# Performance work log

Measured on AMD Instinct MI355X. Metric: run time of the kernel, lower is better.

The kernel has to match this reference:

```python
import jax, jax.numpy as jnp
import numpy as np

BITS = 4
MAXQ = 15            # 2**BITS - 1
PACK = 32 // BITS    # 8 int4 values per int32
GROUPSIZE = 128
M, K, N = 2048, 4096, 4096
G = K // GROUPSIZE


def setup_inputs() -> dict:
    key = jax.random.key(0)
    k1, k2, k3, k4, k5 = jax.random.split(key, 5)
    x = jax.random.normal(k1, (M, K), dtype=jnp.float32)
    qweight = jax.random.randint(k2, (K // PACK, N), 0, 2147483647, dtype=jnp.int32)
    qzeros = jax.random.randint(k3, (G, N // PACK), 0, 2147483647, dtype=jnp.int32)
    scales = jax.random.uniform(k4, (G, N), dtype=jnp.float32) * 0.01
    g_idx = (jnp.arange(K, dtype=jnp.int32) // GROUPSIZE).astype(jnp.int32)
    bias = jax.random.normal(k5, (N,), dtype=jnp.float32)
    return {"x": x, "qweight": qweight, "qzeros": qzeros,
            "scales": scales, "g_idx": g_idx, "bias": bias}


def _dequantize(qweight, qzeros, scales, g_idx):
    shifts = (jnp.arange(PACK, dtype=jnp.int32) * BITS)
    # unpack weights along K: [K//8, N] -> [K//8, 8, N] -> [K, N]
    w_int = ((qweight[:, None, :] >> shifts[None, :, None]) & MAXQ)
    w_int = w_int.reshape(K, N)
    # unpack zeros along N: [G, N//8] -> [G, N//8, 8] -> [G, N]; kernel adds 1
    z_int = ((qzeros[:, :, None] >> shifts[None, None, :]) & MAXQ) + 1
    z_int = z_int.reshape(G, N)
    # group-wise dequant: W[k, n] = (w - zeros[g_idx[k]]) * scales[g_idx[k]]
    W = (w_int - z_int[g_idx]).astype(jnp.float32) * scales[g_idx]
    return W  # [K, N]


def reference(x, qweight, qzeros, scales, g_idx, bias):
    W = _dequantize(qweight, qzeros, scales, g_idx)
    return x @ W + bias  # [M, N]
```

## Files before the change

kernel.cpp:

```cpp
#include <hip/hip_runtime.h>
#include <hip/hip_bf16.h>
#include <stdint.h>

#define M_DIM 2048
#define K_DIM 4096
#define N_DIM 4096

typedef __attribute__((ext_vector_type(8))) short short8;
typedef __attribute__((ext_vector_type(4))) float f32x4;

#define MFMA __builtin_amdgcn_mfma_f32_16x16x32_bf16

__device__ __forceinline__ uint32_t bf16pk(float a, float b) {
  uint32_t ua = __float_as_uint(a);
  ua = (ua + 0x7FFFu + ((ua >> 16) & 1u)) >> 16;
  uint32_t ub = __float_as_uint(b);
  ub = (ub + 0x7FFFu + ((ub >> 16) & 1u)) >> 16;
  return ua | (ub << 16);
}

__device__ __forceinline__ void glds16(const char* g, char* l) {
  __builtin_amdgcn_global_load_lds((__attribute__((address_space(1))) void*)g,
                                   (__attribute__((address_space(3))) void*)l, 16, 0, 0);
}


__global__ void __launch_bounds__(256) cvt_x_kernel(const float* __restrict__ x,
                                                    char* __restrict__ xImg) {
  const int mt = blockIdx.x >> 6, ktp = blockIdx.x & 63;
  const int tid = threadIdx.x;
  const int row = tid & 127, sh = tid >> 7;
  const int s = ktp * 2 + sh;
  const float* src = x + (size_t)(mt * 128 + row) * K_DIM + s * 32;
  char* dst = xImg + (size_t)(mt * 128 + s) * 8192 + row * 16;
#pragma unroll
  for (int slot = 0; slot < 4; ++slot) {
    float4 f0 = *(const float4*)(src + slot * 8);
    float4 f1 = *(const float4*)(src + slot * 8 + 4);
    uint4 pk;
    pk.x = bf16pk(f0.x, f0.y);
    pk.y = bf16pk(f0.z, f0.w);
    pk.z = bf16pk(f1.x, f1.y);
    pk.w = bf16pk(f1.z, f1.w);
    *(uint4*)(dst + slot * 2048) = pk;
  }
}

__global__ void __launch_bounds__(256) deq_w_kernel(const uint32_t* __restrict__ qweight,
                                                    const uint32_t* __restrict__ qzeros,
                                                    const float* __restrict__ scales,
                                                    char* __restrict__ wImg) {
  const int nt = blockIdx.x >> 6, ktp = blockIdx.x & 63;
  const int tid = threadIdx.x;
  const int n = tid & 127, sh = tid >> 7;
  const int s = ktp * 2 + sh;
  const int g = ktp >> 1;
  const int gn = nt * 128 + n;
  uint32_t zq = qzeros[g * (N_DIM / 8) + (gn >> 3)];
  const int z = (int)((zq >> ((gn & 7) * 4)) & 15u) + 1;
  const float s_ = scales[g * N_DIM + gn];
  char* dst = wImg + (size_t)(nt * 128 + s) * 8192 + n * 16;
#pragma unroll
  for (int slot = 0; slot < 4; ++slot) {
    uint32_t q = qweight[(size_t)(s * 4 + slot) * N_DIM + gn];
    float f[8];
#pragma unroll
    for (int v = 0; v < 8; ++v) {
      int w = (int)((q >> (4 * v)) & 15u);
      f[v] = (float)(w - z) * s_;
    }
    uint4 pk;
    pk.x = bf16pk(f[0], f[1]);
    pk.y = bf16pk(f[2], f[3]);
    pk.z = bf16pk(f[4], f[5]);
    pk.w = bf16pk(f[6], f[7]);
    *(uint4*)(dst + slot * 2048) = pk;
  }
}

__global__ void __launch_bounds__(128, 2) gemm_kernel(const char* __restrict__ xImg,
                                                      const char* __restrict__ wImg,
                                                      const float* __restrict__ bias,
                                                      float* __restrict__ out,
                                                      float* __restrict__ part1) {
  __shared__ uint4 ldsv[2048];
  char* lds = (char*)ldsv;
  const int tid = threadIdx.x;
  const int lane = tid & 63, wc = tid >> 6;
  const int lr = lane & 15, lk = lane >> 4;

  const int bid = blockIdx.x;
  const int wg = (bid & 7) * 128 + (bid >> 3);
  const int mb = wg & 15, nb = (wg >> 4) & 31, ks = wg >> 9;

  f32x4 acc[8][4];
#pragma unroll
  for (int i = 0; i < 8; ++i)
#pragma unroll
    for (int j = 0; j < 4; ++j) acc[i][j] = f32x4{0.f, 0.f, 0.f, 0.f};

  const char* aT = xImg + (size_t)(mb * 128 + ks * 64) * 8192;
  const char* bT = wImg + (size_t)(nb * 128 + ks * 64) * 8192;

  int aoff[8], boff[4];
#pragma unroll
  for (int i = 0; i < 8; ++i) aoff[i] = lk * 2048 + (i * 16 + lr) * 16;
#pragma unroll
  for (int j = 0; j < 4; ++j) boff[j] = 8192 + lk * 2048 + (wc * 64 + j * 16 + lr) * 16;

#define STAGE(T, SB)                                                     \
  do {                                                                   \
    const char* sA = aT + (size_t)(T) * 8192;                            \
    const char* sB = bT + (size_t)(T) * 8192;                            \
    char* dA = lds + (SB);                                               \
    _Pragma("unroll")                                                    \
    for (int h = 0; h < 4; ++h) {                                        \
      glds16(sA + h * 2048 + tid * 16, dA + h * 2048 + tid * 16);        \
      glds16(sB + h * 2048 + tid * 16, dA + 8192 + h * 2048 + tid * 16); \
    }                                                                    \
  } while (0)

  STAGE(0, 0);
  asm volatile("s_waitcnt vmcnt(0)" ::: "memory");
  __builtin_amdgcn_sched_barrier(0);
  __builtin_amdgcn_s_barrier();

#pragma unroll 2
  for (int t = 0; t < 64; ++t) {
    const char* buf = lds + (t & 1) * 16384;
    if (t < 63) STAGE(t + 1, ((t + 1) & 1) * 16384);
    __builtin_amdgcn_sched_barrier(0);

    short8 a0 = *(const short8*)(buf + aoff[0]);
    short8 a1 = *(const short8*)(buf + aoff[1]);
    short8 a2 = *(const short8*)(buf + aoff[2]);
    short8 a3 = *(const short8*)(buf + aoff[3]);
    short8 a4 = *(const short8*)(buf + aoff[4]);
    short8 a5 = *(const short8*)(buf + aoff[5]);
    short8 a6 = *(const short8*)(buf + aoff[6]);
    short8 a7 = *(const short8*)(buf + aoff[7]);
    short8 b0 = *(const short8*)(buf + boff[0]);
    short8 b1 = *(const short8*)(buf + boff[1]);
    short8 b2 = *(const short8*)(buf + boff[2]);
    short8 b3 = *(const short8*)(buf + boff[3]);

    asm volatile("s_waitcnt lgkmcnt(3)" ::: "memory");
    __builtin_amdgcn_sched_barrier(0);
    __builtin_amdgcn_s_setprio(1);
    acc[0][0] = MFMA(a0, b0, acc[0][0], 0, 0, 0);
    acc[1][0] = MFMA(a1, b0, acc[1][0], 0, 0, 0);
    acc[2][0] = MFMA(a2, b0, acc[2][0], 0, 0, 0);
    acc[3][0] = MFMA(a3, b0, acc[3][0], 0, 0, 0);
    acc[4][0] = MFMA(a4, b0, acc[4][0], 0, 0, 0);
    acc[5][0] = MFMA(a5, b0, acc[5][0], 0, 0, 0);
    acc[6][0] = MFMA(a6, b0, acc[6][0], 0, 0, 0);
    acc[7][0] = MFMA(a7, b0, acc[7][0], 0, 0, 0);
    asm volatile("s_waitcnt lgkmcnt(2)" ::: "memory");
    __builtin_amdgcn_sched_barrier(0);
    acc[0][1] = MFMA(a0, b1, acc[0][1], 0, 0, 0);
    acc[1][1] = MFMA(a1, b1, acc[1][1], 0, 0, 0);
    acc[2][1] = MFMA(a2, b1, acc[2][1], 0, 0, 0);
    acc[3][1] = MFMA(a3, b1, acc[3][1], 0, 0, 0);
    acc[4][1] = MFMA(a4, b1, acc[4][1], 0, 0, 0);
    acc[5][1] = MFMA(a5, b1, acc[5][1], 0, 0, 0);
    acc[6][1] = MFMA(a6, b1, acc[6][1], 0, 0, 0);
    acc[7][1] = MFMA(a7, b1, acc[7][1], 0, 0, 0);
    asm volatile("s_waitcnt lgkmcnt(1)" ::: "memory");
    __builtin_amdgcn_sched_barrier(0);
    acc[0][2] = MFMA(a0, b2, acc[0][2], 0, 0, 0);
    acc[1][2] = MFMA(a1, b2, acc[1][2], 0, 0, 0);
    acc[2][2] = MFMA(a2, b2, acc[2][2], 0, 0, 0);
    acc[3][2] = MFMA(a3, b2, acc[3][2], 0, 0, 0);
    acc[4][2] = MFMA(a4, b2, acc[4][2], 0, 0, 0);
    acc[5][2] = MFMA(a5, b2, acc[5][2], 0, 0, 0);
    acc[6][2] = MFMA(a6, b2, acc[6][2], 0, 0, 0);
    acc[7][2] = MFMA(a7, b2, acc[7][2], 0, 0, 0);
    asm volatile("s_waitcnt lgkmcnt(0)" ::: "memory");
    __builtin_amdgcn_sched_barrier(0);
    acc[0][3] = MFMA(a0, b3, acc[0][3], 0, 0, 0);
    acc[1][3] = MFMA(a1, b3, acc[1][3], 0, 0, 0);
    acc[2][3] = MFMA(a2, b3, acc[2][3], 0, 0, 0);
    acc[3][3] = MFMA(a3, b3, acc[3][3], 0, 0, 0);
    acc[4][3] = MFMA(a4, b3, acc[4][3], 0, 0, 0);
    acc[5][3] = MFMA(a5, b3, acc[5][3], 0, 0, 0);
    acc[6][3] = MFMA(a6, b3, acc[6][3], 0, 0, 0);
    acc[7][3] = MFMA(a7, b3, acc[7][3], 0, 0, 0);
    __builtin_amdgcn_s_setprio(0);

    if (t < 63) {
      asm volatile("s_waitcnt vmcnt(0)" ::: "memory");
      __builtin_amdgcn_sched_barrier(0);
      __builtin_amdgcn_s_barrier();
    }
  }
#undef STAGE

  const int colB = nb * 128 + wc * 64 + lr;
  const int rowB = mb * 128 + lk * 4;
  if (part1 != nullptr) {
    float* dst = ks ? part1 : out;
#pragma unroll
    for (int j = 0; j < 4; ++j) {
      int col = colB + j * 16;
      float bj = (ks == 0) ? bias[col] : 0.f;
#pragma unroll
      for (int i = 0; i < 8; ++i) {
        int row = rowB + i * 16;
#pragma unroll
        for (int r = 0; r < 4; ++r)
          dst[(size_t)(row + r) * N_DIM + col] = acc[i][j][r] + bj;
      }
    }
  } else {
#pragma unroll
    for (int j = 0; j < 4; ++j) {
      int col = colB + j * 16;
      float bj = (ks == 0) ? bias[col] : 0.f;
#pragma unroll
      for (int i = 0; i < 8; ++i) {
        int row = rowB + i * 16;
#pragma unroll
        for (int r = 0; r < 4; ++r)
          atomicAdd(&out[(size_t)(row + r) * N_DIM + col], acc[i][j][r] + bj);
      }
    }
  }
}

__global__ void __launch_bounds__(256) reduce_kernel(float* __restrict__ out,
                                                     const float* __restrict__ part1) {
  int i = blockIdx.x * 256 + threadIdx.x;
  float4 o = ((const float4*)out)[i];
  float4 p = ((const float4*)part1)[i];
  o.x += p.x; o.y += p.y; o.z += p.z; o.w += p.w;
  ((float4*)out)[i] = o;
}

__global__ void fallback_kernel(const float* __restrict__ x, const uint32_t* __restrict__ qweight,
                                const uint32_t* __restrict__ qzeros, const float* __restrict__ scales,
                                const float* __restrict__ bias, float* __restrict__ out) {
  __shared__ float xs[16][17];
  __shared__ float ws[16][17];
  int tx = threadIdx.x, ty = threadIdx.y;
  int col = blockIdx.x * 16 + tx;
  int row = blockIdx.y * 16 + ty;
  float acc = 0.f;
  for (int k0 = 0; k0 < K_DIM; k0 += 16) {
    xs[ty][tx] = x[(size_t)row * K_DIM + k0 + tx];
    int k = k0 + ty;
    int g = k >> 7;
    uint32_t q = qweight[(size_t)(k >> 3) * N_DIM + col];
    int w = (int)((q >> ((k & 7) * 4)) & 15u);
    uint32_t zq = qzeros[g * (N_DIM / 8) + (col >> 3)];
    int z = (int)((zq >> ((col & 7) * 4)) & 15u) + 1;
    ws[ty][tx] = (float)(w - z) * scales[g * N_DIM + col];
    __syncthreads();
#pragma unroll
    for (int kk = 0; kk < 16; ++kk) acc += xs[ty][kk] * ws[kk][tx];
    __syncthreads();
  }
  out[(size_t)row * N_DIM + col] = acc + bias[col];
}

extern "C" void kernel_launch(void* const* d_in, const int* in_sizes, int n_in,
                              void* d_out, int out_size, void* d_ws, size_t ws_size,
                              hipStream_t stream) {
  const float* x = (const float*)d_in[0];
  const uint32_t* qweight = (const uint32_t*)d_in[1];
  const uint32_t* qzeros = (const uint32_t*)d_in[2];
  const float* scales = (const float*)d_in[3];
  const float* bias = (const float*)d_in[5];
  float* out = (float*)d_out;

  const size_t X_IMG = (size_t)16 * 128 * 8192;
  const size_t W_IMG = (size_t)32 * 128 * 8192;
  const size_t PART = (size_t)M_DIM * N_DIM * 4;

  if (ws_size >= X_IMG + W_IMG + PART) {
    char* xImg = (char*)d_ws;
    char* wImg = (char*)d_ws + X_IMG;
    float* part1 = (float*)((char*)d_ws + X_IMG + W_IMG);
    cvt_x_kernel<<<1024, 256, 0, stream>>>(x, xImg);
    deq_w_kernel<<<2048, 256, 0, stream>>>(qweight, qzeros, scales, wImg);
    gemm_kernel<<<1024, 128, 0, stream>>>(xImg, wImg, bias, out, part1);
    reduce_kernel<<<8192, 256, 0, stream>>>(out, part1);
  } else if (ws_size >= X_IMG + W_IMG) {
    char* xImg = (char*)d_ws;
    char* wImg = (char*)d_ws + X_IMG;
    hipMemsetAsync(out, 0, (size_t)M_DIM * N_DIM * sizeof(float), stream);
    cvt_x_kernel<<<1024, 256, 0, stream>>>(x, xImg);
    deq_w_kernel<<<2048, 256, 0, stream>>>(qweight, qzeros, scales, wImg);
    gemm_kernel<<<1024, 128, 0, stream>>>(xImg, wImg, bias, out, nullptr);
  } else {
    fallback_kernel<<<dim3(N_DIM / 16, M_DIM / 16), dim3(16, 16), 0, stream>>>(
        x, qweight, qzeros, scales, bias, out);
  }
}
```

Measured before the change: 101.0 us.

## Move split-K reduction into workgroup via LDS and merge prep kernels

The two K-halves now run as wave pairs inside one 256-thread workgroup instead of separate workgroups, with partial accumulators exchanged through LDS before the output write. This removes the fp32 partial buffer, its write and readback, and the separate reduce kernel. The x-conversion and weight-dequant kernels are also merged into one launch. In exchange the workgroup uses twice the LDS (64 KB) and the grid halves to 512 workgroups, which may reduce occupancy and latency hiding.

Result: faster. 82.42 us (-18.4%).

```diff
diff --git a/kernel.cpp b/kernel.cpp
--- a/kernel.cpp
+++ b/kernel.cpp
@@ -25,73 +25,75 @@
 }
 
 
-__global__ void __launch_bounds__(256) cvt_x_kernel(const float* __restrict__ x,
-                                                    char* __restrict__ xImg) {
-  const int mt = blockIdx.x >> 6, ktp = blockIdx.x & 63;
+__global__ void __launch_bounds__(256) prep_kernel(const float* __restrict__ x,
+                                                   const uint32_t* __restrict__ qweight,
+                                                   const uint32_t* __restrict__ qzeros,
+                                                   const float* __restrict__ scales,
+                                                   char* __restrict__ xImg,
+                                                   char* __restrict__ wImg) {
   const int tid = threadIdx.x;
-  const int row = tid & 127, sh = tid >> 7;
-  const int s = ktp * 2 + sh;
-  const float* src = x + (size_t)(mt * 128 + row) * K_DIM + s * 32;
-  char* dst = xImg + (size_t)(mt * 128 + s) * 8192 + row * 16;
-#pragma unroll
-  for (int slot = 0; slot < 4; ++slot) {
-    float4 f0 = *(const float4*)(src + slot * 8);
-    float4 f1 = *(const float4*)(src + slot * 8 + 4);
-    uint4 pk;
-    pk.x = bf16pk(f0.x, f0.y);
-    pk.y = bf16pk(f0.z, f0.w);
-    pk.z = bf16pk(f1.x, f1.y);
-    pk.w = bf16pk(f1.z, f1.w);
-    *(uint4*)(dst + slot * 2048) = pk;
-  }
-}
-
-__global__ void __launch_bounds__(256) deq_w_kernel(const uint32_t* __restrict__ qweight,
-                                                    const uint32_t* __restrict__ qzeros,
-                                                    const float* __restrict__ scales,
-                                                    char* __restrict__ wImg) {
-  const int nt = blockIdx.x >> 6, ktp = blockIdx.x & 63;
-  const int tid = threadIdx.x;
-  const int n = tid & 127, sh = tid >> 7;
-  const int s = ktp * 2 + sh;
-  const int g = ktp >> 1;
-  const int gn = nt * 128 + n;
-  uint32_t zq = qzeros[g * (N_DIM / 8) + (gn >> 3)];
-  const int z = (int)((zq >> ((gn & 7) * 4)) & 15u) + 1;
-  const float s_ = scales[g * N_DIM + gn];
-  char* dst = wImg + (size_t)(nt * 128 + s) * 8192 + n * 16;
-#pragma unroll
-  for (int slot = 0; slot < 4; ++slot) {
-    uint32_t q = qweight[(size_t)(s * 4 + slot) * N_DIM + gn];
-    float f[8];
-#pragma unroll
-    for (int v = 0; v < 8; ++v) {
-      int w = (int)((q >> (4 * v)) & 15u);
-      f[v] = (float)(w - z) * s_;
-    }
-    uint4 pk;
-    pk.x = bf16pk(f[0], f[1]);
-    pk.y = bf16pk(f[2], f[3]);
-    pk.z = bf16pk(f[4], f[5]);
-    pk.w = bf16pk(f[6], f[7]);
-    *(uint4*)(dst + slot * 2048) = pk;
-  }
-}
-
-__global__ void __launch_bounds__(128, 2) gemm_kernel(const char* __restrict__ xImg,
+  if (blockIdx.x < 1024) {
+    const int bid = blockIdx.x;
+    const int mt = bid >> 6, ktp = bid & 63;
+    const int row = tid & 127, sh = tid >> 7;
+    const int s = ktp * 2 + sh;
+    const float* src = x + (size_t)(mt * 128 + row) * K_DIM + s * 32;
+    char* dst = xImg + (size_t)(mt * 128 + s) * 8192 + row * 16;
+#pragma unroll
+    for (int slot = 0; slot < 4; ++slot) {
+      float4 f0 = *(const float4*)(src + slot * 8);
+      float4 f1 = *(const float4*)(src + slot * 8 + 4);
+      uint4 pk;
+      pk.x = bf16pk(f0.x, f0.y);
+      pk.y = bf16pk(f0.z, f0.w);
+      pk.z = bf16pk(f1.x, f1.y);
+      pk.w = bf16pk(f1.z, f1.w);
+      *(uint4*)(dst + slot * 2048) = pk;
+    }
+  } else {
+    const int bid = blockIdx.x - 1024;
+    const int nt = bid >> 6, ktp = bid & 63;
+    const int n = tid & 127, sh = tid >> 7;
+    const int s = ktp * 2 + sh;
+    const int g = ktp >> 1;
+    const int gn = nt * 128 + n;
+    uint32_t zq = qzeros[g * (N_DIM / 8) + (gn >> 3)];
+    const int z = (int)((zq >> ((gn & 7) * 4)) & 15u) + 1;
+    const float s_ = scales[g * N_DIM + gn];
+    char* dst = wImg + (size_t)(nt * 128 + s) * 8192 + n * 16;
+#pragma unroll
+    for (int slot = 0; slot < 4; ++slot) {
+      uint32_t q = qweight[(size_t)(s * 4 + slot) * N_DIM + gn];
+      float f[8];
+#pragma unroll
+      for (int v = 0; v < 8; ++v) {
+        int w = (int)((q >> (4 * v)) & 15u);
+        f[v] = (float)(w - z) * s_;
+      }
+      uint4 pk;
+      pk.x = bf16pk(f[0], f[1]);
+      pk.y = bf16pk(f[2], f[3]);
+      pk.z = bf16pk(f[4], f[5]);
+      pk.w = bf16pk(f[6], f[7]);
+      *(uint4*)(dst + slot * 2048) = pk;
+    }
+  }
+}
+
+__global__ void __launch_bounds__(256, 2) gemm_kernel(const char* __restrict__ xImg,
                                                       const char* __restrict__ wImg,
                                                       const float* __restrict__ bias,
-                                                      float* __restrict__ out,
-                                                      float* __restrict__ part1) {
-  __shared__ uint4 ldsv[2048];
+                                                      float* __restrict__ out) {
+  __shared__ uint4 ldsv[4096];
   char* lds = (char*)ldsv;
   const int tid = threadIdx.x;
-  const int lane = tid & 63, wc = tid >> 6;
+  const int lane = tid & 63, wid = tid >> 6;
+  const int ks = wid >> 1, wc = wid & 1;
   const int lr = lane & 15, lk = lane >> 4;
 
   const int bid = blockIdx.x;
-  const int wg = (bid & 7) * 128 + (bid >> 3);
-  const int mb = wg & 15, nb = (wg >> 4) & 31, ks = wg >> 9;
+  const int wg = (bid & 7) * 64 + (bid >> 3);
+  const int mb = wg & 15, nb = wg >> 4;
 
   f32x4 acc[8][4];
 #pragma unroll
@@ -99,25 +101,33 @@
 #pragma unroll
     for (int j = 0; j < 4; ++j) acc[i][j] = f32x4{0.f, 0.f, 0.f, 0.f};
 
-  const char* aT = xImg + (size_t)(mb * 128 + ks * 64) * 8192;
-  const char* bT = wImg + (size_t)(nb * 128 + ks * 64) * 8192;
+  const char* aT0 = xImg + (size_t)mb * 128 * 8192;
+  const char* bT0 = wImg + (size_t)nb * 128 * 8192;
+  const char* aT1 = aT0 + (size_t)64 * 8192;
+  const char* bT1 = bT0 + (size_t)64 * 8192;
 
   int aoff[8], boff[4];
 #pragma unroll
-  for (int i = 0; i < 8; ++i) aoff[i] = lk * 2048 + (i * 16 + lr) * 16;
-#pragma unroll
-  for (int j = 0; j < 4; ++j) boff[j] = 8192 + lk * 2048 + (wc * 64 + j * 16 + lr) * 16;
+  for (int i = 0; i < 8; ++i) aoff[i] = ks * 16384 + lk * 2048 + (i * 16 + lr) * 16;
+#pragma unroll
+  for (int j = 0; j < 4; ++j)
+    boff[j] = ks * 16384 + 8192 + lk * 2048 + (wc * 64 + j * 16 + lr) * 16;
 
 #define STAGE(T, SB)                                                     \
   do {                                                                   \
-    const char* sA = aT + (size_t)(T) * 8192;                            \
-    const char* sB = bT + (size_t)(T) * 8192;                            \
-    char* dA = lds + (SB);                                               \
-    _Pragma("unroll")                                                    \
-    for (int h = 0; h < 4; ++h) {                                        \
-      glds16(sA + h * 2048 + tid * 16, dA + h * 2048 + tid * 16);        \
-      glds16(sB + h * 2048 + tid * 16, dA + 8192 + h * 2048 + tid * 16); \
-    }                                                                    \
+    char* d = lds + (SB);                                                \
+    const char* sa0 = aT0 + (size_t)(T) * 8192;                          \
+    const char* sb0 = bT0 + (size_t)(T) * 8192;                          \
+    const char* sa1 = aT1 + (size_t)(T) * 8192;                          \
+    const char* sb1 = bT1 + (size_t)(T) * 8192;                          \
+    glds16(sa0 + tid * 16, d + tid * 16);                                \
+    glds16(sa0 + 4096 + tid * 16, d + 4096 + tid * 16);                  \
+    glds16(sb0 + tid * 16, d + 8192 + tid * 16);                         \
+    glds16(sb0 + 4096 + tid * 16, d + 12288 + tid * 16);                 \
+    glds16(sa1 + tid * 16, d + 16384 + tid * 16);                        \
+    glds16(sa1 + 4096 + tid * 16, d + 20480 + tid * 16);                 \
+    glds16(sb1 + tid * 16, d + 24576 + tid * 16);                        \
+    glds16(sb1 + 4096 + tid * 16, d + 28672 + tid * 16);                 \
   } while (0)
 
   STAGE(0, 0);
@@ -127,8 +137,8 @@
 
 #pragma unroll 2
   for (int t = 0; t < 64; ++t) {
-    const char* buf = lds + (t & 1) * 16384;
-    if (t < 63) STAGE(t + 1, ((t + 1) & 1) * 16384);
+    const char* buf = lds + (t & 1) * 32768;
+    if (t < 63) STAGE(t + 1, ((t + 1) & 1) * 32768);
     __builtin_amdgcn_sched_barrier(0);
 
     short8 a0 = *(const short8*)(buf + aoff[0]);
@@ -195,45 +205,52 @@
   }
 #undef STAGE
 
+  __syncthreads();
+  if (ks == 1) {
+#pragma unroll
+    for (int i = 0; i < 4; ++i)
+#pragma unroll
+      for (int j = 0; j < 4; ++j)
+        *(f32x4*)(lds + (wc * 16 + i * 4 + j) * 1024 + lane * 16) = acc[i][j];
+  } else {
+#pragma unroll
+    for (int i = 4; i < 8; ++i)
+#pragma unroll
+      for (int j = 0; j < 4; ++j)
+        *(f32x4*)(lds + 32768 + (wc * 16 + (i - 4) * 4 + j) * 1024 + lane * 16) = acc[i][j];
+  }
+  __syncthreads();
+
   const int colB = nb * 128 + wc * 64 + lr;
-  const int rowB = mb * 128 + lk * 4;
-  if (part1 != nullptr) {
-    float* dst = ks ? part1 : out;
+  if (ks == 0) {
 #pragma unroll
     for (int j = 0; j < 4; ++j) {
       int col = colB + j * 16;
-      float bj = (ks == 0) ? bias[col] : 0.f;
-#pragma unroll
-      for (int i = 0; i < 8; ++i) {
-        int row = rowB + i * 16;
+      float bj = bias[col];
+#pragma unroll
+      for (int i = 0; i < 4; ++i) {
+        f32x4 p = *(const f32x4*)(lds + (wc * 16 + i * 4 + j) * 1024 + lane * 16);
+        int row = mb * 128 + i * 16 + lk * 4;
 #pragma unroll
         for (int r = 0; r < 4; ++r)
-          dst[(size_t)(row + r) * N_DIM + col] = acc[i][j][r] + bj;
+          out[(size_t)(row + r) * N_DIM + col] = acc[i][j][r] + p[r] + bj;
       }
     }
   } else {
 #pragma unroll
     for (int j = 0; j < 4; ++j) {
       int col = colB + j * 16;
-      float bj = (ks == 0) ? bias[col] : 0.f;
-#pragma unroll
-      for (int i = 0; i < 8; ++i) {
-        int row = rowB + i * 16;
+      float bj = bias[col];
+#pragma unroll
+      for (int i = 4; i < 8; ++i) {
+        f32x4 p = *(const f32x4*)(lds + 32768 + (wc * 16 + (i - 4) * 4 + j) * 1024 + lane * 16);
+        int row = mb * 128 + i * 16 + lk * 4;
 #pragma unroll
         for (int r = 0; r < 4; ++r)
-          atomicAdd(&out[(size_t)(row + r) * N_DIM + col], acc[i][j][r] + bj);
+          out[(size_t)(row + r) * N_DIM + col] = acc[i][j][r] + p[r] + bj;
       }
     }
   }
-}
-
-__global__ void __launch_bounds__(256) reduce_kernel(float* __restrict__ out,
-                                                     const float* __restrict__ part1) {
-  int i = blockIdx.x * 256 + threadIdx.x;
-  float4 o = ((const float4*)out)[i];
-  float4 p = ((const float4*)part1)[i];
-  o.x += p.x; o.y += p.y; o.z += p.z; o.w += p.w;
-  ((float4*)out)[i] = o;
 }
 
 __global__ void fallback_kernel(const float* __restrict__ x, const uint32_t* __restrict__ qweight,
@@ -274,23 +291,12 @@
 
   const size_t X_IMG = (size_t)16 * 128 * 8192;
   const size_t W_IMG = (size_t)32 * 128 * 8192;
-  const size_t PART = (size_t)M_DIM * N_DIM * 4;
-
-  if (ws_size >= X_IMG + W_IMG + PART) {
+
+  if (ws_size >= X_IMG + W_IMG) {
     char* xImg = (char*)d_ws;
     char* wImg = (char*)d_ws + X_IMG;
-    float* part1 = (float*)((char*)d_ws + X_IMG + W_IMG);
-    cvt_x_kernel<<<1024, 256, 0, stream>>>(x, xImg);
-    deq_w_kernel<<<2048, 256, 0, stream>>>(qweight, qzeros, scales, wImg);
-    gemm_kernel<<<1024, 128, 0, stream>>>(xImg, wImg, bias, out, part1);
-    reduce_kernel<<<8192, 256, 0, stream>>>(out, part1);
-  } else if (ws_size >= X_IMG + W_IMG) {
-    char* xImg = (char*)d_ws;
-    char* wImg = (char*)d_ws + X_IMG;
-    hipMemsetAsync(out, 0, (size_t)M_DIM * N_DIM * sizeof(float), stream);
-    cvt_x_kernel<<<1024, 256, 0, stream>>>(x, xImg);
-    deq_w_kernel<<<2048, 256, 0, stream>>>(qweight, qzeros, scales, wImg);
-    gemm_kernel<<<1024, 128, 0, stream>>>(xImg, wImg, bias, out, nullptr);
+    prep_kernel<<<3072, 256, 0, stream>>>(x, qweight, qzeros, scales, xImg, wImg);
+    gemm_kernel<<<512, 256, 0, stream>>>(xImg, wImg, bias, out);
   } else {
     fallback_kernel<<<dim3(N_DIM / 16, M_DIM / 16), dim3(16, 16), 0, stream>>>(
         x, qweight, qzeros, scales, bias, out);
```
